# Kernel optimization log

Hardware: AMD Instinct MI355X
Metric: run time of the kernel (lower is better)

Reference implementation:

```python
import jax, jax.numpy as jnp
import numpy as np

B_SZ, C_IN, H, W = 2, 96, 128, 128
DT_RANK, D_STATE, D_INNER = 8, 16, 96


def pscan2d(A, X):
    """Faithful port of PScan2DUnified.forward / pscan2d_optimized.

    A, X: (b, H, W, d, N). The source's downsweep writes into index_select
    COPIES (discarded in torch), so the effective computation is the upsweep
    only: at level k (stride s=2**k), for each 2x2 block of active elements,
    X[dst] += A[dst] * X[src]; A[dst] *= A[src], where src=(s-1::2s, s-1::2s)
    and dst=(2s-1::2s, 2s-1::2s). Requires H, W powers of two.
    """
    h, w = A.shape[1], A.shape[2]
    K = min(int(np.log2(h)), int(np.log2(w)))
    for k in range(K):
        s = 2 ** k
        Asrc = A[:, s - 1::2 * s, s - 1::2 * s]
        Xsrc = X[:, s - 1::2 * s, s - 1::2 * s]
        Adst = A[:, 2 * s - 1::2 * s, 2 * s - 1::2 * s]
        X = X.at[:, 2 * s - 1::2 * s, 2 * s - 1::2 * s].add(Adst * Xsrc)
        A = A.at[:, 2 * s - 1::2 * s, 2 * s - 1::2 * s].multiply(Asrc)
    return X


def setup_inputs() -> dict:
    key = jax.random.key(0)
    ks = jax.random.split(key, 5)
    x = jax.random.normal(ks[0], (B_SZ, C_IN, H, W), dtype=jnp.float32)
    # 1x1 conv weights stored as (out, in) matrices
    deltaBC_w = jax.random.normal(ks[1], (DT_RANK + 2 * D_STATE, C_IN), dtype=jnp.float32) * 0.02
    deltaBC_b = jnp.zeros((DT_RANK + 2 * D_STATE,), dtype=jnp.float32)
    dt_w = jax.random.normal(ks[2], (D_INNER, DT_RANK), dtype=jnp.float32) * 0.02
    dt_b = jnp.zeros((D_INNER,), dtype=jnp.float32)
    # faithful init: log(linspace(1,2,N)) repeated over d_inner
    A_log = jnp.tile(jnp.log(jnp.linspace(1.0, 2.0, D_STATE, dtype=jnp.float32)), (D_INNER, 1))
    D = jnp.ones((D_INNER,), dtype=jnp.float32)
    return {"x": x, "deltaBC_w": deltaBC_w, "deltaBC_b": deltaBC_b,
            "dt_w": dt_w, "dt_b": dt_b, "A_log": A_log, "D": D}


def reference(x, deltaBC_w, deltaBC_b, dt_w, dt_b, A_log, D):
    A = -jnp.exp(A_log)  # (d, N)
    # 1x1 conv == per-pixel matmul
    dBC = jnp.einsum('bchw,oc->bohw', x, deltaBC_w) + deltaBC_b[None, :, None, None]
    delta = dBC[:, :DT_RANK]
    Bm = dBC[:, DT_RANK:DT_RANK + D_STATE]
    Cm = dBC[:, DT_RANK + D_STATE:]
    delta = jax.nn.softplus(jnp.einsum('bchw,oc->bohw', delta, dt_w) + dt_b[None, :, None, None])
    delta = delta.transpose(0, 2, 3, 1)   # (b,H,W,d)
    Bm = Bm.transpose(0, 2, 3, 1)         # (b,H,W,N)
    Cm = Cm.transpose(0, 2, 3, 1)         # (b,H,W,N)
    xh = x.transpose(0, 2, 3, 1)          # (b,H,W,d)
    A_bar = jnp.exp(delta[..., None] * A)                         # (b,H,W,d,N)
    BX = (delta[..., None] * Bm[:, :, :, None, :]) * xh[..., None]  # (b,H,W,d,N)
    hs = pscan2d(A_bar, BX)                                       # (b,H,W,d,N)
    y = jnp.einsum('bhwdn,bhwn->bhwd', hs, Cm) + D * xh
    return y
```

## Files before the change

### kernel.cpp

```cpp
#include <hip/hip_runtime.h>
#include <cstdint>

#define CIN 96
#define DIN 96
#define DTR 8
#define DST 16
#define HH 128
#define WW 128
#define HW (HH*WW)
#define NPIX (2*HW)
#define DIAG (WW+1)
#define LOG2E 1.4426950408889634f

__device__ __forceinline__ float softplus_f(float t) {
    return (t > 20.0f) ? t : __logf(1.0f + __expf(t));
}

__device__ __forceinline__ void load_An(const float* __restrict__ AwsT, int d, float* An) {
    float4 A0 = *reinterpret_cast<const float4*>(AwsT + d * 16);
    float4 A1 = *reinterpret_cast<const float4*>(AwsT + d * 16 + 4);
    float4 A2 = *reinterpret_cast<const float4*>(AwsT + d * 16 + 8);
    float4 A3 = *reinterpret_cast<const float4*>(AwsT + d * 16 + 12);
    An[0]=A0.x; An[1]=A0.y; An[2]=A0.z; An[3]=A0.w;
    An[4]=A1.x; An[5]=A1.y; An[6]=A1.z; An[7]=A1.w;
    An[8]=A2.x; An[9]=A2.y; An[10]=A2.z; An[11]=A2.w;
    An[12]=A3.x; An[13]=A3.y; An[14]=A3.z; An[15]=A3.w;
}

__device__ __forceinline__ float c_dot(const float* __restrict__ rc, const float* acc16) {
    float4 C0 = *reinterpret_cast<const float4*>(rc);
    float4 C1 = *reinterpret_cast<const float4*>(rc + 4);
    float4 C2 = *reinterpret_cast<const float4*>(rc + 8);
    float4 C3 = *reinterpret_cast<const float4*>(rc + 12);
    float ys = 0.f;
    ys = fmaf(acc16[0],C0.x,ys); ys = fmaf(acc16[1],C0.y,ys);
    ys = fmaf(acc16[2],C0.z,ys); ys = fmaf(acc16[3],C0.w,ys);
    ys = fmaf(acc16[4],C1.x,ys); ys = fmaf(acc16[5],C1.y,ys);
    ys = fmaf(acc16[6],C1.z,ys); ys = fmaf(acc16[7],C1.w,ys);
    ys = fmaf(acc16[8],C2.x,ys); ys = fmaf(acc16[9],C2.y,ys);
    ys = fmaf(acc16[10],C2.z,ys); ys = fmaf(acc16[11],C2.w,ys);
    ys = fmaf(acc16[12],C3.x,ys); ys = fmaf(acc16[13],C3.y,ys);
    ys = fmaf(acc16[14],C3.z,ys); ys = fmaf(acc16[15],C3.w,ys);
    return ys;
}

__global__ __launch_bounds__(512) void ssm2d_dbc(
    const float* __restrict__ x,
    const float* __restrict__ W1, const float* __restrict__ b1,
    const float* __restrict__ dtw, const float* __restrict__ dtb,
    const float* __restrict__ alog, const float* __restrict__ Dv,
    float* __restrict__ bc, float2* __restrict__ dc,
    float* __restrict__ Aws, float* __restrict__ out)
{
    __shared__ float sX[CIN][65];
    __shared__ float sOut[64][41];
    __shared__ float sDelta[DIN][65];
    __shared__ float sAn[DIN][17];
    __shared__ float sBC[64];

    const int t = threadIdx.x;
    const int blk = blockIdx.x;
    const int b = blk >> 8;
    const int tile = blk & 255;
    const int a = tile >> 2;
    const int b2 = tile & 3;
    const int r0 = a << 1;
    const int c0 = b2 << 5;
    const float* xb = x + (size_t)b * CIN * HW;

    #pragma unroll
    for (int it = 0; it < 3; ++it) {
        int i4 = it * 512 + t;
        int ch = i4 >> 4;
        int px4 = (i4 & 15) << 2;
        int row = r0 + (px4 >> 5);
        int col = c0 + (px4 & 31);
        float4 v = *reinterpret_cast<const float4*>(xb + (size_t)ch * HW + row * WW + col);
        sX[ch][px4 + 0] = v.x; sX[ch][px4 + 1] = v.y;
        sX[ch][px4 + 2] = v.z; sX[ch][px4 + 3] = v.w;
    }
    for (int i = t; i < DIN * DST; i += 512) {
        float v = -__expf(alog[i]) * LOG2E;
        sAn[i >> 4][i & 15] = v;
        if (blk == 0) Aws[i] = v;
    }
    __syncthreads();

    const int lane = t & 63;
    const int w = __builtin_amdgcn_readfirstlane(t >> 6);
    const int og = w * 5;
    float a0 = b1[og + 0], a1 = b1[og + 1], a2 = b1[og + 2],
          a3 = b1[og + 3], a4 = b1[og + 4];
    #pragma unroll 16
    for (int ch = 0; ch < CIN; ++ch) {
        float xv = sX[ch][lane];
        a0 = fmaf(xv, W1[(og + 0) * CIN + ch], a0);
        a1 = fmaf(xv, W1[(og + 1) * CIN + ch], a1);
        a2 = fmaf(xv, W1[(og + 2) * CIN + ch], a2);
        a3 = fmaf(xv, W1[(og + 3) * CIN + ch], a3);
        a4 = fmaf(xv, W1[(og + 4) * CIN + ch], a4);
    }
    sOut[lane][og + 0] = a0; sOut[lane][og + 1] = a1; sOut[lane][og + 2] = a2;
    sOut[lane][og + 3] = a3; sOut[lane][og + 4] = a4;
    __syncthreads();

    if (t < 64) {
        float s = 0.f;
        #pragma unroll
        for (int n = 0; n < DST; ++n) s += sOut[t][8 + n] * sOut[t][24 + n];
        sBC[t] = s;
    }
    __syncthreads();

    #pragma unroll
    for (int it = 0; it < 12; ++it) {
        int i = it * 512 + t;
        int px = i / 96;
        int d = i - px * 96;
        float tt = dtb[d];
        float4 wA = *reinterpret_cast<const float4*>(dtw + d * DTR);
        float4 wB = *reinterpret_cast<const float4*>(dtw + d * DTR + 4);
        tt = fmaf(sOut[px][0], wA.x, tt); tt = fmaf(sOut[px][1], wA.y, tt);
        tt = fmaf(sOut[px][2], wA.z, tt); tt = fmaf(sOut[px][3], wA.w, tt);
        tt = fmaf(sOut[px][4], wB.x, tt); tt = fmaf(sOut[px][5], wB.y, tt);
        tt = fmaf(sOut[px][6], wB.z, tt); tt = fmaf(sOut[px][7], wB.w, tt);
        float delta = softplus_f(tt);
        float xv = sX[d][px];
        sDelta[d][px] = delta;
        int rg = r0 + (px >> 5), cg = c0 + (px & 31);
        size_t pg = (size_t)b * HW + rg * WW + cg;
        out[pg * 96 + d] = xv * fmaf(delta, sBC[px], Dv[d]);
        if (((rg - cg) & 3) == 0)
            dc[pg * 96 + d] = make_float2(delta, delta * xv);
    }
    #pragma unroll
    for (int it = 0; it < 4; ++it) {
        int i = it * 512 + t;
        int px = i >> 5;
        int n = i & 31;
        int rg = r0 + (px >> 5), cg = c0 + (px & 31);
        if (((rg - cg) & 3) == 0) {
            size_t pg = (size_t)b * HW + rg * WW + cg;
            bc[pg * 32 + n] = sOut[px][8 + n];
        }
    }
    __syncthreads();

    for (int ii = t; ii < 16 * 96; ii += 512) {
        int k = ii / 96;
        int d = ii - k * 96;
        bool live = !((a & 1) && (k & 1));
        int pxd = 33 + 2 * k;
        int anc = 2 * k;
        float ddst = sDelta[d][pxd];
        float ca = sDelta[d][anc] * sX[d][anc];
        float y = 0.f;
        #pragma unroll
        for (int n = 0; n < 16; ++n)
            y = fmaf(sOut[pxd][24 + n] * exp2f(sAn[d][n] * ddst) * sOut[anc][8 + n], ca, y);
        if (live) {
            int rg = r0 + 1, cg = c0 + 1 + 2 * k;
            size_t g = ((size_t)b * HW + rg * WW + cg) * 96 + d;
            out[g] += y;
        }
    }
}

template<int M>
__device__ __forceinline__ void decode_item(int e, int& p, int& d, bool& live) {
    d = e % 96;
    int pxi = e / 96;
    const int sh = 7 - M;
    const int nM = 1 << sh;
    const int half = nM * nM;
    int img = pxi >= half;
    int e2 = pxi - (img ? half : 0);
    int rr = e2 >> sh;
    int cc = e2 & (nM - 1);
    live = ((rr & cc & 1) == 0);
    int r = ((rr + 1) << M) - 1;
    int c = ((cc + 1) << M) - 1;
    p = img * HW + r * WW + c;
}

template<int L>
__device__ __forceinline__ void chain_LT(int p, int d, bool live,
    const float* __restrict__ bc, const float2* __restrict__ dc,
    const float* __restrict__ AwsT, float* __restrict__ out)
{
    size_t base = (size_t)p * 96 + d;
    float2 v0 = dc[base];
    float2 vj[L - 1];
    #pragma unroll
    for (int j = 1; j < L; ++j)
        vj[j - 1] = dc[(size_t)(p - j * DIAG) * 96 + d];
    float An[16];
    load_An(AwsT, d, An);
    float acc16[16];
    #pragma unroll
    for (int n = 0; n < 16; ++n) acc16[n] = 0.f;
    float S = v0.x;
    #pragma unroll
    for (int j = 1; j < L; ++j) {
        const float* rb = bc + (size_t)(p - j * DIAG) * 32;
        float4 B0 = *reinterpret_cast<const float4*>(rb);
        float4 B1 = *reinterpret_cast<const float4*>(rb + 4);
        float4 B2 = *reinterpret_cast<const float4*>(rb + 8);
        float4 B3 = *reinterpret_cast<const float4*>(rb + 12);
        float Bv[16] = {B0.x,B0.y,B0.z,B0.w, B1.x,B1.y,B1.z,B1.w,
                        B2.x,B2.y,B2.z,B2.w, B3.x,B3.y,B3.z,B3.w};
        float cj = vj[j - 1].y;
        #pragma unroll
        for (int n = 0; n < 16; ++n)
            acc16[n] = fmaf(exp2f(An[n] * S) * Bv[n], cj, acc16[n]);
        S += vj[j - 1].x;
    }
    float ys = c_dot(bc + (size_t)p * 32 + 16, acc16);
    if (live) out[base] += ys;
}

__device__ __forceinline__ void chain_RT(int p, int d, int L, bool live,
    const float* __restrict__ bc, const float2* __restrict__ dc,
    const float* __restrict__ AwsT, float* __restrict__ out)
{
    size_t base = (size_t)p * 96 + d;
    float An[16];
    load_An(AwsT, d, An);
    float acc16[16];
    #pragma unroll
    for (int n = 0; n < 16; ++n) acc16[n] = 0.f;
    float S = dc[base].x;
    int pj = p;
    for (int j = 1; j < L; ++j) {
        pj -= DIAG;
        float2 v = dc[(size_t)pj * 96 + d];
        const float* rb = bc + (size_t)pj * 32;
        float4 B0 = *reinterpret_cast<const float4*>(rb);
        float4 B1 = *reinterpret_cast<const float4*>(rb + 4);
        float4 B2 = *reinterpret_cast<const float4*>(rb + 8);
        float4 B3 = *reinterpret_cast<const float4*>(rb + 12);
        float Bv[16] = {B0.x,B0.y,B0.z,B0.w, B1.x,B1.y,B1.z,B1.w,
                        B2.x,B2.y,B2.z,B2.w, B3.x,B3.y,B3.z,B3.w};
        #pragma unroll
        for (int n = 0; n < 16; ++n)
            acc16[n] = fmaf(exp2f(An[n] * S) * Bv[n], v.y, acc16[n]);
        S += v.x;
    }
    float ys = c_dot(bc + (size_t)p * 32 + 16, acc16);
    if (live) out[base] += ys;
}

#define K2_M2 768
#define K2_M3 192
#define K2_M4 48
#define K2_LONG 768
__global__ __launch_bounds__(256) void ssm2d_scan(
    const float* __restrict__ bc, const float2* __restrict__ dc,
    const float* __restrict__ AwsT, float* __restrict__ out)
{
    const int t = threadIdx.x;
    const int blk = blockIdx.x;

    if (blk < K2_M2) {
        int e = blk * 256 + t;
        int p, d; bool live;
        decode_item<2>(e, p, d, live);
        chain_LT<4>(p, d, live, bc, dc, AwsT, out);
    } else if (blk < K2_M2 + K2_M3) {
        int e = (blk - K2_M2) * 256 + t;
        int p, d; bool live;
        decode_item<3>(e, p, d, live);
        chain_RT(p, d, 8, live, bc, dc, AwsT, out);
    } else if (blk < K2_M2 + K2_M3 + K2_M4) {
        int e = (blk - K2_M2 - K2_M3) * 256 + t;
        int p, d; bool live;
        decode_item<4>(e, p, d, live);
        chain_RT(p, d, 16, live, bc, dc, AwsT, out);
    } else {
        const int wv = t >> 6;
        const int lane = t & 63;
        int waveid = (blk - (K2_M2 + K2_M3 + K2_M4)) * 4 + wv;
        int pix = waveid / DIN;
        int d = waveid - pix * DIN;
        int batch = pix >> 4;
        int sel = pix & 15;
        int r = ((sel >> 2) + 1) * 32 - 1;
        int c = ((sel & 3) + 1) * 32 - 1;
        int p = batch * HW + r * WW + c;
        int m = __builtin_ctz(r + 1);
        int mc = __builtin_ctz(c + 1);
        if (mc < m) m = mc;
        int L = 1 << m;

        float An[16];
        load_An(AwsT, d, An);
        float acc16[16];
        #pragma unroll
        for (int n = 0; n < 16; ++n) acc16[n] = 0.0f;
        float Scarry = 0.0f;

        for (int jb = 0; jb < L; jb += 64) {
            int j = jb + lane;
            bool act = (j < L);
            int jc = act ? j : 0;
            int pj = p - DIAG * jc;
            float2 v = dc[(size_t)pj * 96 + d];
            float dj = act ? v.x : 0.0f;
            float cj = (j >= 1 && act) ? v.y : 0.0f;

            float incl = dj;
            #pragma unroll
            for (int off = 1; off < 64; off <<= 1) {
                float u = __shfl_up(incl, off);
                if (lane >= off) incl += u;
            }
            float S = Scarry + incl - dj;

            const float* rb = bc + (size_t)pj * 32;
            float4 B0 = *reinterpret_cast<const float4*>(rb);
            float4 B1 = *reinterpret_cast<const float4*>(rb + 4);
            float4 B2 = *reinterpret_cast<const float4*>(rb + 8);
            float4 B3 = *reinterpret_cast<const float4*>(rb + 12);
            float Bv[16] = {B0.x,B0.y,B0.z,B0.w, B1.x,B1.y,B1.z,B1.w,
                            B2.x,B2.y,B2.z,B2.w, B3.x,B3.y,B3.z,B3.w};
            #pragma unroll
            for (int n = 0; n < 16; ++n)
                acc16[n] = fmaf(exp2f(An[n] * S) * Bv[n], cj, acc16[n]);

            Scarry += __shfl(incl, 63);
        }

        #pragma unroll
        for (int off = 32; off >= 1; off >>= 1) {
            #pragma unroll
            for (int n = 0; n < 16; ++n) acc16[n] += __shfl_xor(acc16[n], off);
        }

        if (lane == 0) {
            float y = c_dot(bc + (size_t)p * 32 + 16, acc16);
            out[(size_t)p * 96 + d] += y;
        }
    }
}

extern "C" void kernel_launch(void* const* d_in, const int* in_sizes, int n_in,
                              void* d_out, int out_size, void* d_ws, size_t ws_size,
                              hipStream_t stream) {
    const float* x    = (const float*)d_in[0];
    const float* W1   = (const float*)d_in[1];
    const float* b1   = (const float*)d_in[2];
    const float* dtw  = (const float*)d_in[3];
    const float* dtb  = (const float*)d_in[4];
    const float* alog = (const float*)d_in[5];
    const float* Dv   = (const float*)d_in[6];
    float* out = (float*)d_out;

    char* ws = (char*)d_ws;
    float2* dc  = (float2*)(ws);
    float*  bcb = (float*)(ws + 25165824);
    float*  Aws = (float*)(ws + 29360128);

    hipLaunchKernelGGL(ssm2d_dbc, dim3(512), dim3(512), 0, stream,
                       x, W1, b1, dtw, dtb, alog, Dv,
                       bcb, dc, Aws, out);
    hipLaunchKernelGGL(ssm2d_scan, dim3(K2_M2 + K2_M3 + K2_M4 + K2_LONG), dim3(256), 0, stream,
                       bcb, dc, Aws, out);
}
```

Measured before the change: 39.74 us.

## Reshape first-kernel tiles to 4x16 and fold level-2 scan chains into it

```diff
diff --git a/kernel.cpp b/kernel.cpp
--- a/kernel.cpp
+++ b/kernel.cpp
@@ -62,22 +62,23 @@
     const int blk = blockIdx.x;
     const int b = blk >> 8;
     const int tile = blk & 255;
-    const int a = tile >> 2;
-    const int b2 = tile & 3;
-    const int r0 = a << 1;
-    const int c0 = b2 << 5;
+    const int a = tile >> 3;
+    const int b2 = tile & 7;
+    const int r0 = a << 2;
+    const int c0 = b2 << 4;
     const float* xb = x + (size_t)b * CIN * HW;
 
     #pragma unroll
     for (int it = 0; it < 3; ++it) {
         int i4 = it * 512 + t;
         int ch = i4 >> 4;
-        int px4 = (i4 & 15) << 2;
-        int row = r0 + (px4 >> 5);
-        int col = c0 + (px4 & 31);
-        float4 v = *reinterpret_cast<const float4*>(xb + (size_t)ch * HW + row * WW + col);
-        sX[ch][px4 + 0] = v.x; sX[ch][px4 + 1] = v.y;
-        sX[ch][px4 + 2] = v.z; sX[ch][px4 + 3] = v.w;
+        int sub = i4 & 15;
+        int row = sub >> 2;
+        int col4 = (sub & 3) << 2;
+        float4 v = *reinterpret_cast<const float4*>(xb + (size_t)ch * HW + (r0 + row) * WW + c0 + col4);
+        int px = row * 16 + col4;
+        sX[ch][px + 0] = v.x; sX[ch][px + 1] = v.y;
+        sX[ch][px + 2] = v.z; sX[ch][px + 3] = v.w;
     }
     for (int i = t; i < DIN * DST; i += 512) {
         float v = -__expf(alog[i]) * LOG2E;
@@ -127,10 +128,10 @@
         float delta = softplus_f(tt);
         float xv = sX[d][px];
         sDelta[d][px] = delta;
-        int rg = r0 + (px >> 5), cg = c0 + (px & 31);
+        int rg = r0 + (px >> 4), cg = c0 + (px & 15);
         size_t pg = (size_t)b * HW + rg * WW + cg;
         out[pg * 96 + d] = xv * fmaf(delta, sBC[px], Dv[d]);
-        if (((rg - cg) & 3) == 0)
+        if (((rg - cg) & 7) == 0)
             dc[pg * 96 + d] = make_float2(delta, delta * xv);
     }
     #pragma unroll
@@ -138,8 +139,8 @@
         int i = it * 512 + t;
         int px = i >> 5;
         int n = i & 31;
-        int rg = r0 + (px >> 5), cg = c0 + (px & 31);
-        if (((rg - cg) & 3) == 0) {
+        int rg = r0 + (px >> 4), cg = c0 + (px & 15);
+        if (((rg - cg) & 7) == 0) {
             size_t pg = (size_t)b * HW + rg * WW + cg;
             bc[pg * 32 + n] = sOut[px][8 + n];
         }
@@ -147,19 +148,36 @@
     __syncthreads();
 
     for (int ii = t; ii < 16 * 96; ii += 512) {
-        int k = ii / 96;
-        int d = ii - k * 96;
-        bool live = !((a & 1) && (k & 1));
-        int pxd = 33 + 2 * k;
-        int anc = 2 * k;
-        float ddst = sDelta[d][pxd];
-        float ca = sDelta[d][anc] * sX[d][anc];
+        int oi = ii / 96;
+        int d = ii - oi * 96;
+        int row, col, L;
+        bool live = true;
+        if (oi < 8)       { row = 1; col = 2 * oi + 1; L = 2; }
+        else if (oi < 12) { row = 3; col = 4 * (oi - 8) + 1; L = 2; }
+        else              { row = 3; col = 4 * (oi - 12) + 3; L = 4;
+                            live = !((a & 1) && ((oi - 12) & 1)); }
+        int pxd = row * 16 + col;
+        float An[16];
+        #pragma unroll
+        for (int n = 0; n < 16; ++n) An[n] = sAn[d][n];
+        float acc[16];
+        #pragma unroll
+        for (int n = 0; n < 16; ++n) acc[n] = 0.f;
+        float S = sDelta[d][pxd];
+        for (int s = 1; s < L; ++s) {
+            int aix = pxd - 17 * s;
+            float da = sDelta[d][aix];
+            float ca = da * sX[d][aix];
+            #pragma unroll
+            for (int n = 0; n < 16; ++n)
+                acc[n] = fmaf(exp2f(An[n] * S) * sOut[aix][8 + n], ca, acc[n]);
+            S += da;
+        }
         float y = 0.f;
         #pragma unroll
-        for (int n = 0; n < 16; ++n)
-            y = fmaf(sOut[pxd][24 + n] * exp2f(sAn[d][n] * ddst) * sOut[anc][8 + n], ca, y);
+        for (int n = 0; n < 16; ++n) y = fmaf(acc[n], sOut[pxd][24 + n], y);
         if (live) {
-            int rg = r0 + 1, cg = c0 + 1 + 2 * k;
+            int rg = r0 + row, cg = c0 + col;
             size_t g = ((size_t)b * HW + rg * WW + cg) * 96 + d;
             out[g] += y;
         }
@@ -181,42 +199,6 @@
     int r = ((rr + 1) << M) - 1;
     int c = ((cc + 1) << M) - 1;
     p = img * HW + r * WW + c;
-}
-
-template<int L>
-__device__ __forceinline__ void chain_LT(int p, int d, bool live,
-    const float* __restrict__ bc, const float2* __restrict__ dc,
-    const float* __restrict__ AwsT, float* __restrict__ out)
-{
-    size_t base = (size_t)p * 96 + d;
-    float2 v0 = dc[base];
-    float2 vj[L - 1];
-    #pragma unroll
-    for (int j = 1; j < L; ++j)
-        vj[j - 1] = dc[(size_t)(p - j * DIAG) * 96 + d];
-    float An[16];
-    load_An(AwsT, d, An);
-    float acc16[16];
-    #pragma unroll
-    for (int n = 0; n < 16; ++n) acc16[n] = 0.f;
-    float S = v0.x;
-    #pragma unroll
-    for (int j = 1; j < L; ++j) {
-        const float* rb = bc + (size_t)(p - j * DIAG) * 32;
-        float4 B0 = *reinterpret_cast<const float4*>(rb);
-        float4 B1 = *reinterpret_cast<const float4*>(rb + 4);
-        float4 B2 = *reinterpret_cast<const float4*>(rb + 8);
-        float4 B3 = *reinterpret_cast<const float4*>(rb + 12);
-        float Bv[16] = {B0.x,B0.y,B0.z,B0.w, B1.x,B1.y,B1.z,B1.w,
-                        B2.x,B2.y,B2.z,B2.w, B3.x,B3.y,B3.z,B3.w};
-        float cj = vj[j - 1].y;
-        #pragma unroll
-        for (int n = 0; n < 16; ++n)
-            acc16[n] = fmaf(exp2f(An[n] * S) * Bv[n], cj, acc16[n]);
-        S += vj[j - 1].x;
-    }
-    float ys = c_dot(bc + (size_t)p * 32 + 16, acc16);
-    if (live) out[base] += ys;
 }
 
 __device__ __forceinline__ void chain_RT(int p, int d, int L, bool live,
@@ -250,7 +232,6 @@
     if (live) out[base] += ys;
 }
 
-#define K2_M2 768
 #define K2_M3 192
 #define K2_M4 48
 #define K2_LONG 768
@@ -261,25 +242,20 @@
     const int t = threadIdx.x;
     const int blk = blockIdx.x;
 
-    if (blk < K2_M2) {
+    if (blk < K2_M3) {
         int e = blk * 256 + t;
-        int p, d; bool live;
-        decode_item<2>(e, p, d, live);
-        chain_LT<4>(p, d, live, bc, dc, AwsT, out);
-    } else if (blk < K2_M2 + K2_M3) {
-        int e = (blk - K2_M2) * 256 + t;
         int p, d; bool live;
         decode_item<3>(e, p, d, live);
         chain_RT(p, d, 8, live, bc, dc, AwsT, out);
-    } else if (blk < K2_M2 + K2_M3 + K2_M4) {
-        int e = (blk - K2_M2 - K2_M3) * 256 + t;
+    } else if (blk < K2_M3 + K2_M4) {
+        int e = (blk - K2_M3) * 256 + t;
         int p, d; bool live;
         decode_item<4>(e, p, d, live);
         chain_RT(p, d, 16, live, bc, dc, AwsT, out);
     } else {
         const int wv = t >> 6;
         const int lane = t & 63;
-        int waveid = (blk - (K2_M2 + K2_M3 + K2_M4)) * 4 + wv;
+        int waveid = (blk - (K2_M3 + K2_M4)) * 4 + wv;
         int pix = waveid / DIN;
         int d = waveid - pix * DIN;
         int batch = pix >> 4;
@@ -363,6 +339,6 @@
     hipLaunchKernelGGL(ssm2d_dbc, dim3(512), dim3(512), 0, stream,
                        x, W1, b1, dtw, dtb, alog, Dv,
                        bcb, dc, Aws, out);
-    hipLaunchKernelGGL(ssm2d_scan, dim3(K2_M2 + K2_M3 + K2_M4 + K2_LONG), dim3(256), 0, stream,
+    hipLaunchKernelGGL(ssm2d_scan, dim3(K2_M3 + K2_M4 + K2_LONG), dim3(256), 0, stream,
                        bcb, dc, Aws, out);
 }
```

After: 43.25 us. 8.8% more time.

## Store scan workspace in diagonal-major compact layout for contiguous chain reads

Applied to the files above, without the earlier changes.

```diff
diff --git a/kernel.cpp b/kernel.cpp
--- a/kernel.cpp
+++ b/kernel.cpp
@@ -9,8 +9,9 @@
 #define WW 128
 #define HW (HH*WW)
 #define NPIX (2*HW)
-#define DIAG (WW+1)
 #define LOG2E 1.4426950408889634f
+#define NDIAG 63
+#define DSLOT 128
 
 __device__ __forceinline__ float softplus_f(float t) {
     return (t > 20.0f) ? t : __logf(1.0f + __expf(t));
@@ -130,8 +131,12 @@
         int rg = r0 + (px >> 5), cg = c0 + (px & 31);
         size_t pg = (size_t)b * HW + rg * WW + cg;
         out[pg * 96 + d] = xv * fmaf(delta, sBC[px], Dv[d]);
-        if (((rg - cg) & 3) == 0)
-            dc[pg * 96 + d] = make_float2(delta, delta * xv);
+        if (((rg - cg) & 3) == 0) {
+            int td = ((rg - cg) >> 2) + 31;
+            int jd = (rg < cg) ? rg : cg;
+            size_t row = (size_t)(b * NDIAG + td) * DSLOT + jd;
+            dc[row * 96 + d] = make_float2(delta, delta * xv);
+        }
     }
     #pragma unroll
     for (int it = 0; it < 4; ++it) {
@@ -140,8 +145,10 @@
         int n = i & 31;
         int rg = r0 + (px >> 5), cg = c0 + (px & 31);
         if (((rg - cg) & 3) == 0) {
-            size_t pg = (size_t)b * HW + rg * WW + cg;
-            bc[pg * 32 + n] = sOut[px][8 + n];
+            int td = ((rg - cg) >> 2) + 31;
+            int jd = (rg < cg) ? rg : cg;
+            size_t row = (size_t)(b * NDIAG + td) * DSLOT + jd;
+            bc[row * 32 + n] = sOut[px][8 + n];
         }
     }
     __syncthreads();
@@ -167,7 +174,8 @@
 }
 
 template<int M>
-__device__ __forceinline__ void decode_item(int e, int& p, int& d, bool& live) {
+__device__ __forceinline__ void decode_item(int e, size_t& obase, size_t& drow,
+                                            int& d, bool& live) {
     d = e % 96;
     int pxi = e / 96;
     const int sh = 7 - M;
@@ -180,20 +188,22 @@
     live = ((rr & cc & 1) == 0);
     int r = ((rr + 1) << M) - 1;
     int c = ((cc + 1) << M) - 1;
-    p = img * HW + r * WW + c;
+    obase = ((size_t)(img * HW + r * WW + c)) * 96 + d;
+    int td = ((r - c) >> 2) + 31;
+    int jd = (r < c) ? r : c;
+    drow = (size_t)(img * NDIAG + td) * DSLOT + jd;
 }
 
 template<int L>
-__device__ __forceinline__ void chain_LT(int p, int d, bool live,
+__device__ __forceinline__ void chain_LT(size_t obase, size_t drow, int d, bool live,
     const float* __restrict__ bc, const float2* __restrict__ dc,
     const float* __restrict__ AwsT, float* __restrict__ out)
 {
-    size_t base = (size_t)p * 96 + d;
-    float2 v0 = dc[base];
+    float2 v0 = dc[drow * 96 + d];
     float2 vj[L - 1];
     #pragma unroll
     for (int j = 1; j < L; ++j)
-        vj[j - 1] = dc[(size_t)(p - j * DIAG) * 96 + d];
+        vj[j - 1] = dc[(drow - j) * 96 + d];
     float An[16];
     load_An(AwsT, d, An);
     float acc16[16];
@@ -202,7 +212,7 @@
     float S = v0.x;
     #pragma unroll
     for (int j = 1; j < L; ++j) {
-        const float* rb = bc + (size_t)(p - j * DIAG) * 32;
+        const float* rb = bc + (drow - j) * 32;
         float4 B0 = *reinterpret_cast<const float4*>(rb);
         float4 B1 = *reinterpret_cast<const float4*>(rb + 4);
         float4 B2 = *reinterpret_cast<const float4*>(rb + 8);
@@ -215,26 +225,23 @@
             acc16[n] = fmaf(exp2f(An[n] * S) * Bv[n], cj, acc16[n]);
         S += vj[j - 1].x;
     }
-    float ys = c_dot(bc + (size_t)p * 32 + 16, acc16);
-    if (live) out[base] += ys;
-}
-
-__device__ __forceinline__ void chain_RT(int p, int d, int L, bool live,
+    float ys = c_dot(bc + drow * 32 + 16, acc16);
+    if (live) out[obase] += ys;
+}
+
+__device__ __forceinline__ void chain_RT(size_t obase, size_t drow, int d, int L, bool live,
     const float* __restrict__ bc, const float2* __restrict__ dc,
     const float* __restrict__ AwsT, float* __restrict__ out)
 {
-    size_t base = (size_t)p * 96 + d;
     float An[16];
     load_An(AwsT, d, An);
     float acc16[16];
     #pragma unroll
     for (int n = 0; n < 16; ++n) acc16[n] = 0.f;
-    float S = dc[base].x;
-    int pj = p;
+    float S = dc[drow * 96 + d].x;
     for (int j = 1; j < L; ++j) {
-        pj -= DIAG;
-        float2 v = dc[(size_t)pj * 96 + d];
-        const float* rb = bc + (size_t)pj * 32;
+        float2 v = dc[(drow - j) * 96 + d];
+        const float* rb = bc + (drow - j) * 32;
         float4 B0 = *reinterpret_cast<const float4*>(rb);
         float4 B1 = *reinterpret_cast<const float4*>(rb + 4);
         float4 B2 = *reinterpret_cast<const float4*>(rb + 8);
@@ -246,8 +253,8 @@
             acc16[n] = fmaf(exp2f(An[n] * S) * Bv[n], v.y, acc16[n]);
         S += v.x;
     }
-    float ys = c_dot(bc + (size_t)p * 32 + 16, acc16);
-    if (live) out[base] += ys;
+    float ys = c_dot(bc + drow * 32 + 16, acc16);
+    if (live) out[obase] += ys;
 }
 
 #define K2_M2 768
@@ -263,19 +270,19 @@
 
     if (blk < K2_M2) {
         int e = blk * 256 + t;
-        int p, d; bool live;
-        decode_item<2>(e, p, d, live);
-        chain_LT<4>(p, d, live, bc, dc, AwsT, out);
+        size_t obase, drow; int d; bool live;
+        decode_item<2>(e, obase, drow, d, live);
+        chain_LT<4>(obase, drow, d, live, bc, dc, AwsT, out);
     } else if (blk < K2_M2 + K2_M3) {
         int e = (blk - K2_M2) * 256 + t;
-        int p, d; bool live;
-        decode_item<3>(e, p, d, live);
-        chain_RT(p, d, 8, live, bc, dc, AwsT, out);
+        size_t obase, drow; int d; bool live;
+        decode_item<3>(e, obase, drow, d, live);
+        chain_RT(obase, drow, d, 8, live, bc, dc, AwsT, out);
     } else if (blk < K2_M2 + K2_M3 + K2_M4) {
         int e = (blk - K2_M2 - K2_M3) * 256 + t;
-        int p, d; bool live;
-        decode_item<4>(e, p, d, live);
-        chain_RT(p, d, 16, live, bc, dc, AwsT, out);
+        size_t obase, drow; int d; bool live;
+        decode_item<4>(e, obase, drow, d, live);
+        chain_RT(obase, drow, d, 16, live, bc, dc, AwsT, out);
     } else {
         const int wv = t >> 6;
         const int lane = t & 63;
@@ -292,6 +299,10 @@
         if (mc < m) m = mc;
         int L = 1 << m;
 
+        int td = ((r - c) >> 2) + 31;
+        int jd = (r < c) ? r : c;
+        size_t drow = (size_t)(batch * NDIAG + td) * DSLOT + jd;
+
         float An[16];
         load_An(AwsT, d, An);
         float acc16[16];
@@ -303,8 +314,8 @@
             int j = jb + lane;
             bool act = (j < L);
             int jc = act ? j : 0;
-            int pj = p - DIAG * jc;
-            float2 v = dc[(size_t)pj * 96 + d];
+            size_t prow = drow - jc;
+            float2 v = dc[prow * 96 + d];
             float dj = act ? v.x : 0.0f;
             float cj = (j >= 1 && act) ? v.y : 0.0f;
 
@@ -316,7 +327,7 @@
             }
             float S = Scarry + incl - dj;
 
-            const float* rb = bc + (size_t)pj * 32;
+            const float* rb = bc + prow * 32;
             float4 B0 = *reinterpret_cast<const float4*>(rb);
             float4 B1 = *reinterpret_cast<const float4*>(rb + 4);
             float4 B2 = *reinterpret_cast<const float4*>(rb + 8);
@@ -337,7 +348,7 @@
         }
 
         if (lane == 0) {
-            float y = c_dot(bc + (size_t)p * 32 + 16, acc16);
+            float y = c_dot(bc + drow * 32 + 16, acc16);
             out[(size_t)p * 96 + d] += y;
         }
     }
@@ -357,8 +368,8 @@
 
     char* ws = (char*)d_ws;
     float2* dc  = (float2*)(ws);
-    float*  bcb = (float*)(ws + 25165824);
-    float*  Aws = (float*)(ws + 29360128);
+    float*  bcb = (float*)(ws + 12582912);
+    float*  Aws = (float*)(ws + 14680064);
 
     hipLaunchKernelGGL(ssm2d_dbc, dim3(512), dim3(512), 0, stream,
                        x, W1, b1, dtw, dtb, alog, Dv,
```

Measured after the change: 37.10 us (median of 4 runs). 1.07x faster.
